# Performance work log

Measured on AMD Instinct MI355X. Metric: run time of the kernel, lower is better.

The kernel has to match this reference:

```python
import jax, jax.numpy as jnp
import numpy as np

N_SAMPLES = (16, 16)  # n_samples per layer (layer_specs)
N_MP = 2
N_HEAD = 4
BATCH = 512
N_NODES = 200000
MAX_DEG = 32
FEAT_DIM = 128
PREP_DIM = 128
HEAD_OUT = 64
ATT_HID = 128


def _agg_layer(x, nb, Wa1, wa2, Wx, Wn):
    # x: [m, d] self feats; nb: [m, S, d] neighbor feats
    # Wa1: [H, 2d, K], wa2: [H, K], Wx/Wn: [H, d, o]
    cat = jnp.concatenate([jnp.broadcast_to(x[:, None, :], nb.shape), nb], axis=-1)  # [m,S,2d]
    h = jnp.tanh(jnp.einsum('msd,hdk->mshk', cat, Wa1))          # [m,S,H,K]
    score = jnp.einsum('mshk,hk->mhs', h, wa2)                   # [m,H,S]
    alpha = jax.nn.softmax(score, axis=-1)
    agg = jnp.einsum('mhs,msd->mhd', alpha, nb)                  # [m,H,d]
    out = jax.nn.relu(jnp.einsum('md,hdo->mho', x, Wx) + jnp.einsum('mhd,hdo->mho', agg, Wn))
    return out.reshape(x.shape[0], -1)                           # concat heads -> [m, H*o]


def setup_inputs() -> dict:
    key = jax.random.key(0)
    ks = jax.random.split(key, 12)
    inp = {}
    inp['ids'] = jax.random.randint(ks[0], (BATCH,), 0, N_NODES, dtype=jnp.int32)
    inp['feats'] = jax.random.normal(ks[1], (N_NODES, FEAT_DIM), dtype=jnp.float32)
    inp['adjs'] = jax.random.randint(ks[2], (N_MP, N_NODES, MAX_DEG), 0, N_NODES, dtype=jnp.int32)
    inp['W_prep'] = jax.random.normal(ks[3], (FEAT_DIM, PREP_DIM), dtype=jnp.float32) / np.sqrt(FEAT_DIM)
    d0, d1 = PREP_DIM, N_HEAD * HEAD_OUT  # layer input dims: 128, 256
    inp['Watt1_0'] = jax.random.normal(ks[4], (N_MP, N_HEAD, 2 * d0, ATT_HID), dtype=jnp.float32) / np.sqrt(2 * d0)
    inp['watt2_0'] = jax.random.normal(ks[5], (N_MP, N_HEAD, ATT_HID), dtype=jnp.float32) / np.sqrt(ATT_HID)
    inp['Wx_0'] = jax.random.normal(ks[6], (N_MP, N_HEAD, d0, HEAD_OUT), dtype=jnp.float32) / np.sqrt(d0)
    inp['Wn_0'] = jax.random.normal(ks[7], (N_MP, N_HEAD, d0, HEAD_OUT), dtype=jnp.float32) / np.sqrt(d0)
    inp['Watt1_1'] = jax.random.normal(ks[8], (N_MP, N_HEAD, 2 * d1, ATT_HID), dtype=jnp.float32) / np.sqrt(2 * d1)
    inp['watt2_1'] = jax.random.normal(ks[9], (N_MP, N_HEAD, ATT_HID), dtype=jnp.float32) / np.sqrt(ATT_HID)
    inp['Wx_1'] = jax.random.normal(ks[10], (N_MP, N_HEAD, d1, HEAD_OUT), dtype=jnp.float32) / np.sqrt(d1)
    inp['Wn_1'] = jax.random.normal(ks[11], (N_MP, N_HEAD, d1, HEAD_OUT), dtype=jnp.float32) / np.sqrt(d1)
    return inp


def reference(ids, feats, adjs, W_prep, Watt1_0, watt2_0, Wx_0, Wn_0, Watt1_1, watt2_1, Wx_1, Wn_1):
    # eval mode (train=False): dropouts are identity
    init = feats[ids] @ W_prep  # prep(ids, feats[ids]) -> [B, 128]
    params = ((Watt1_0, watt2_0, Wx_0, Wn_0), (Watt1_1, watt2_1, Wx_1, Wn_1))
    outs = []
    for mp in range(N_MP):
        adj = adjs[mp]
        cur = ids
        all_feats = [init]
        # neighbor sampling + gather per layer (frontier: 512 -> 8192 -> 131072)
        for li, S in enumerate(N_SAMPLES):
            k = jax.random.fold_in(jax.random.key(42), mp * 16 + li)
            cols = jax.random.randint(k, (cur.shape[0], S), 0, MAX_DEG)
            cur = adj[cur[:, None], cols].reshape(-1)
            all_feats.append(feats[cur] @ W_prep)
        # depth aggregation: each layer collapses the frontier list by one level
        for li, (Wa1, wa2, Wx, Wn) in enumerate(params):
            new_feats = []
            for k_ in range(len(all_feats) - 1):
                x = all_feats[k_]
                nb = all_feats[k_ + 1].reshape(x.shape[0], N_SAMPLES[k_], -1)
                new_feats.append(_agg_layer(x, nb, Wa1[mp], wa2[mp], Wx[mp], Wn[mp]))
            all_feats = new_feats
        assert len(all_feats) == 1
        outs.append(all_feats[0])
    return jnp.stack(outs)  # [n_mp, B, n_head*head_out] = [2, 512, 256]
```

## Files before the change

kernel.cpp:

```cpp
#include <hip/hip_runtime.h>
#include <math.h>


typedef __attribute__((ext_vector_type(8))) short bf16x8;
typedef __attribute__((ext_vector_type(4))) float f32x4;

__device__ __forceinline__ float b2f(unsigned short u) {
  union { unsigned u; float f; } c; c.u = ((unsigned)u) << 16; return c.f;
}
__device__ __forceinline__ unsigned short f2b(float f) {
  union { float f; unsigned u; } c; c.f = f;
  return (unsigned short)((c.u + 0x7FFFu + ((c.u >> 16) & 1u)) >> 16);
}

__device__ __forceinline__ float fast_tanh_pre(float x) {
  float z; asm("v_exp_f32 %0, %1" : "=v"(z) : "v"(x));
  float zp1 = z + 1.f;
  float w; asm("v_rcp_f32 %0, %1" : "=v"(w) : "v"(zp1));
  return fmaf(-2.f, w, 1.f);
}
__device__ __forceinline__ float fast_exp(float x) {
  float y = x * 1.4426950408889634f;
  float z; asm("v_exp_f32 %0, %1" : "=v"(z) : "v"(y));
  return z;
}

__host__ __device__ __forceinline__ void tf2x32(unsigned k0, unsigned k1,
                                                unsigned x0, unsigned x1,
                                                unsigned& o0, unsigned& o1) {
  const unsigned ks2 = k0 ^ k1 ^ 0x1BD11BDAu;
  unsigned v0 = x0 + k0, v1 = x1 + k1;
#define TFR(r) { v0 += v1; v1 = (v1 << (r)) | (v1 >> (32 - (r))); v1 ^= v0; }
  TFR(13) TFR(15) TFR(26) TFR(6)
  v0 += k1;  v1 += ks2 + 1u;
  TFR(17) TFR(29) TFR(16) TFR(24)
  v0 += ks2; v1 += k0 + 2u;
  TFR(13) TFR(15) TFR(26) TFR(6)
  v0 += k0;  v1 += k1 + 3u;
  TFR(17) TFR(29) TFR(16) TFR(24)
  v0 += k1;  v1 += ks2 + 4u;
  TFR(13) TFR(15) TFR(26) TFR(6)
  v0 += ks2; v1 += k0 + 5u;
#undef TFR
  o0 = v0; o1 = v1;
}

__global__ void frontier2_kernel(const int* __restrict__ adjs,
                                 const int* __restrict__ ids,
                                 int* __restrict__ nodes_all,
                                 unsigned a00, unsigned a01, unsigned b00, unsigned b01,
                                 unsigned a10, unsigned a11, unsigned b10, unsigned b11) {
  const int mp = blockIdx.z;
  const int* adj = adjs + (size_t)mp * 6400000;
  int* nodes = nodes_all + (size_t)mp * 139776;
  unsigned k0a = mp ? a10 : a00, k1a = mp ? a11 : a01;
  unsigned k0b = mp ? b10 : b00, k1b = mp ? b11 : b01;
  int i = blockIdx.x * 256 + threadIdx.x;
  int j = i >> 4;
  unsigned y0, y1;
  tf2x32(k0a, k1a, 0u, (unsigned)j, y0, y1);
  int col1 = (int)((y0 ^ y1) & 31u);
  int p0 = ids[j >> 4];
  int f1 = adj[(size_t)p0 * 32 + col1];
  tf2x32(k0b, k1b, 0u, (unsigned)i, y0, y1);
  int col2 = (int)((y0 ^ y1) & 31u);
  int f2 = adj[(size_t)f1 * 32 + col2];
  nodes[8704 + i] = f2;
  if ((i & 15) == 0) nodes[512 + j] = f1;
  if (i < 512) nodes[i] = ids[i];
}

__global__ void transcast_kernel(const float* __restrict__ Wp,
                                 const float* __restrict__ Wa1_0,
                                 const float* __restrict__ Wa1_1,
                                 const float* __restrict__ Wx_0,
                                 const float* __restrict__ Wn_0,
                                 const float* __restrict__ Wx_1,
                                 const float* __restrict__ Wn_1,
                                 unsigned short* __restrict__ Wpt) {
  const float TS = 2.8853900817779268f;
  int o = blockIdx.x * 256 + threadIdx.x;
  if (o >= 1196032) return;
  float v;
  if (o < 16384) {
    int k = o & 127, c = o >> 7;
    v = Wp[k * 128 + c];
  } else if (o < 278528) {
    int o2 = o - 16384;
    int k = o2 & 127, c = (o2 >> 7) & 127, h = (o2 >> 14) & 3,
        half = (o2 >> 16) & 1, mpi = o2 >> 17;
    v = TS * Wa1_0[(((size_t)(mpi * 4 + h) * 256) + half * 128 + k) * 128 + c];
  } else if (o < 802816) {
    int o3 = o - 278528;
    int k = o3 & 255, c = (o3 >> 8) & 127, h = (o3 >> 15) & 3,
        half = (o3 >> 17) & 1, mpi = o3 >> 18;
    v = TS * Wa1_1[(((size_t)(mpi * 4 + h) * 512) + half * 256 + k) * 128 + c];
  } else if (o < 868352) {
    int o4 = o - 802816;
    int k = o4 & 127, oo = (o4 >> 7) & 63, h = (o4 >> 13) & 3, mpi = o4 >> 15;
    v = Wx_0[(((size_t)(mpi * 4 + h) * 128) + k) * 64 + oo];
  } else if (o < 933888) {
    int o4 = o - 868352;
    int k = o4 & 127, oo = (o4 >> 7) & 63, h = (o4 >> 13) & 3, mpi = o4 >> 15;
    v = Wn_0[(((size_t)(mpi * 4 + h) * 128) + k) * 64 + oo];
  } else if (o < 1064960) {
    int o5 = o - 933888;
    int k = o5 & 255, oo = (o5 >> 8) & 63, h = (o5 >> 14) & 3, mpi = o5 >> 16;
    v = Wx_1[(((size_t)(mpi * 4 + h) * 256) + k) * 64 + oo];
  } else {
    int o5 = o - 1064960;
    int k = o5 & 255, oo = (o5 >> 8) & 63, h = (o5 >> 14) & 3, mpi = o5 >> 16;
    v = Wn_1[(((size_t)(mpi * 4 + h) * 256) + k) * 64 + oo];
  }
  Wpt[o] = f2b(v);
}

template <int MODE, bool A_F32, int NKS, int MG>
__global__ __launch_bounds__(256) void mfma_gemm(
    const void* __restrict__ Av, const int* __restrict__ gather,
    const unsigned short* __restrict__ WT, void* __restrict__ Cv,
    int ldc, int mclamp, int a_str, int g_str, int w_str, int c_str) {
  constexpr int K = NKS * 32;
  const int t = threadIdx.x;
  const int w = t >> 6, l = t & 63;
  const int lr = l & 15, lg = l >> 4;
  const int hb = blockIdx.y;
  const int mp = blockIdx.z;
  const int rbase = blockIdx.x * (4 * MG * 16) + w * (MG * 16);

  const unsigned short* Wb = WT + (size_t)mp * w_str + (size_t)hb * 128 * K;
  f32x4 acc[MG][8] = {};

  int arow[MG];
#pragma unroll
  for (int mg = 0; mg < MG; ++mg) {
    int row = rbase + mg * 16 + lr;
    arow[mg] = gather ? gather[(size_t)mp * g_str + row] : min(row, mclamp);
  }
  const float* Af = (const float*)Av;
  const unsigned short* Ab = ((const unsigned short*)Av) + (size_t)mp * a_str;

#pragma unroll
  for (int ks = 0; ks < NKS; ++ks) {
    const int koff = ks * 32 + lg * 8;
    bf16x8 a[MG], b[8];
#pragma unroll
    for (int mg = 0; mg < MG; ++mg) {
      if (A_F32) {
        const float* p = Af + (size_t)arow[mg] * K + koff;
        float4 v0 = *(const float4*)p;
        float4 v1 = *(const float4*)(p + 4);
        union { short s[8]; bf16x8 v; } u;
        u.s[0] = (short)f2b(v0.x); u.s[1] = (short)f2b(v0.y);
        u.s[2] = (short)f2b(v0.z); u.s[3] = (short)f2b(v0.w);
        u.s[4] = (short)f2b(v1.x); u.s[5] = (short)f2b(v1.y);
        u.s[6] = (short)f2b(v1.z); u.s[7] = (short)f2b(v1.w);
        a[mg] = u.v;
      } else {
        a[mg] = *(const bf16x8*)(Ab + (size_t)arow[mg] * K + koff);
      }
    }
#pragma unroll
    for (int f = 0; f < 8; ++f)
      b[f] = *(const bf16x8*)(Wb + (size_t)(f * 16 + lr) * K + koff);
#pragma unroll
    for (int mg = 0; mg < MG; ++mg)
#pragma unroll
      for (int f = 0; f < 8; ++f)
        acc[mg][f] = __builtin_amdgcn_mfma_f32_16x16x32_bf16(a[mg], b[f], acc[mg][f], 0, 0, 0);
  }

  if (MODE == 0) {
    unsigned short* Cb = ((unsigned short*)Cv) + (size_t)mp * c_str;
#pragma unroll
    for (int mg = 0; mg < MG; ++mg)
#pragma unroll
      for (int f = 0; f < 8; ++f)
#pragma unroll
        for (int r = 0; r < 4; ++r)
          Cb[(size_t)(rbase + mg * 16 + lg * 4 + r) * ldc + f * 16 + lr] =
              f2b(acc[mg][f][r]);
  } else {
    float* Cf = ((float*)Cv) + (size_t)mp * c_str;
#pragma unroll
    for (int mg = 0; mg < MG; ++mg)
#pragma unroll
      for (int f = 0; f < 8; ++f)
#pragma unroll
        for (int r = 0; r < 4; ++r)
          Cf[(size_t)(rbase + mg * 16 + lg * 4 + r) * ldc + hb * 128 + f * 16 + lr] =
              acc[mg][f][r];
  }
}

template <int NKS, int MG>
__global__ __launch_bounds__(256, 2) void aggsc_mfma(
    const unsigned short* __restrict__ NB, const int* __restrict__ gather,
    const float* __restrict__ Tb, const unsigned short* __restrict__ WTbot,
    const float* __restrict__ wa2, unsigned short* __restrict__ AG,
    int nb_str, int g_str, int t_str, int w_str, int wa2_str, int ag_str) {
  constexpr int K = NKS * 32;
  constexpr int KP = K + 8;
  constexpr int ROWS = MG * 16;
  const int t = threadIdx.x;
  const int w = t >> 6, l = t & 63;
  const int lr = l & 15, lg = l >> 4;
  const int mp = blockIdx.z;
  const int rbase = blockIdx.x * ROWS;

  __shared__ unsigned short NBs[ROWS * KP];
  __shared__ float alsh[4][MG][16];

  const unsigned short* NBm = NB + (size_t)mp * nb_str;
  const int* gm = gather ? gather + (size_t)mp * g_str : nullptr;

  constexpr int CH = (ROWS * K) / (256 * 8);
#pragma unroll
  for (int q = 0; q < CH; ++q) {
    int c = q * 256 + t;
    int row = c / (K / 8), kc = c % (K / 8);
    int src = gm ? gm[rbase + row] : (rbase + row);
    bf16x8 v = *(const bf16x8*)(NBm + (size_t)src * K + kc * 8);
    *(bf16x8*)(&NBs[row * KP + kc * 8]) = v;
  }
  __syncthreads();

  const unsigned short* Wb = WTbot + (size_t)mp * w_str + (size_t)w * 128 * K;
  float sc[MG][4];
#pragma unroll
  for (int mg = 0; mg < MG; ++mg)
#pragma unroll
    for (int r = 0; r < 4; ++r) sc[mg][r] = 0.f;

#pragma unroll 1
  for (int half = 0; half < 2; ++half) {
    f32x4 acc[MG][4] = {};
#pragma unroll
    for (int ks = 0; ks < NKS; ++ks) {
      const int koff = ks * 32 + lg * 8;
      bf16x8 a[MG], b[4];
#pragma unroll
      for (int f = 0; f < 4; ++f)
        b[f] = *(const bf16x8*)(Wb + (size_t)(half * 64 + f * 16 + lr) * K + koff);
#pragma unroll
      for (int mg = 0; mg < MG; ++mg)
        a[mg] = *(const bf16x8*)(&NBs[(mg * 16 + lr) * KP + koff]);
#pragma unroll
      for (int mg = 0; mg < MG; ++mg)
#pragma unroll
        for (int f = 0; f < 4; ++f)
          acc[mg][f] = __builtin_amdgcn_mfma_f32_16x16x32_bf16(a[mg], b[f], acc[mg][f], 0, 0, 0);
    }
    float w2h[4];
#pragma unroll
    for (int f = 0; f < 4; ++f)
      w2h[f] = wa2[(size_t)mp * wa2_str + w * 128 + half * 64 + f * 16 + lr];
#pragma unroll
    for (int mg = 0; mg < MG; ++mg) {
      const int i = blockIdx.x * MG + mg;
      float tvh[4];
#pragma unroll
      for (int f = 0; f < 4; ++f)
        tvh[f] = Tb[(size_t)mp * t_str + (size_t)i * 512 + w * 128 + half * 64 + f * 16 + lr];
#pragma unroll
      for (int r = 0; r < 4; ++r) {
        float s = 0.f;
#pragma unroll
        for (int f = 0; f < 4; ++f)
          s += fast_tanh_pre(acc[mg][f][r] + tvh[f]) * w2h[f];
        sc[mg][r] += s;
      }
    }
  }

#pragma unroll
  for (int mg = 0; mg < MG; ++mg) {
    float s0 = sc[mg][0], s1 = sc[mg][1], s2 = sc[mg][2], s3 = sc[mg][3];
    s0 += __shfl_xor(s0, 1); s0 += __shfl_xor(s0, 2); s0 += __shfl_xor(s0, 4); s0 += __shfl_xor(s0, 8);
    s1 += __shfl_xor(s1, 1); s1 += __shfl_xor(s1, 2); s1 += __shfl_xor(s1, 4); s1 += __shfl_xor(s1, 8);
    s2 += __shfl_xor(s2, 1); s2 += __shfl_xor(s2, 2); s2 += __shfl_xor(s2, 4); s2 += __shfl_xor(s2, 8);
    s3 += __shfl_xor(s3, 1); s3 += __shfl_xor(s3, 2); s3 += __shfl_xor(s3, 4); s3 += __shfl_xor(s3, 8);
    float mx = fmaxf(fmaxf(s0, s1), fmaxf(s2, s3));
    mx = fmaxf(mx, __shfl_xor(mx, 16));
    mx = fmaxf(mx, __shfl_xor(mx, 32));
    float e0 = fast_exp(s0 - mx), e1 = fast_exp(s1 - mx);
    float e2 = fast_exp(s2 - mx), e3 = fast_exp(s3 - mx);
    float sum = e0 + e1 + e2 + e3;
    sum += __shfl_xor(sum, 16); sum += __shfl_xor(sum, 32);
    float inv = 1.f / sum;
    if (lr == 0) {
      alsh[w][mg][lg * 4 + 0] = e0 * inv;
      alsh[w][mg][lg * 4 + 1] = e1 * inv;
      alsh[w][mg][lg * 4 + 2] = e2 * inv;
      alsh[w][mg][lg * 4 + 3] = e3 * inv;
    }
  }

  constexpr int NCH = K >> 7;
#pragma unroll
  for (int mg = 0; mg < MG; ++mg) {
    const int i = blockIdx.x * MG + mg;
    float al[16];
#pragma unroll
    for (int s = 0; s < 16; ++s) al[s] = alsh[w][mg][s];
#pragma unroll
    for (int c = 0; c < NCH; ++c) {
      const int d = l * 2 + c * 128;
      float a0 = 0.f, a1 = 0.f;
#pragma unroll
      for (int s = 0; s < 16; ++s) {
        unsigned v = *(const unsigned*)(&NBs[(mg * 16 + s) * KP + d]);
        a0 = fmaf(al[s], b2f((unsigned short)(v & 0xffffu)), a0);
        a1 = fmaf(al[s], b2f((unsigned short)(v >> 16)), a1);
      }
      unsigned o = (unsigned)f2b(a0) | ((unsigned)f2b(a1) << 16);
      *(unsigned*)(AG + (size_t)mp * ag_str + ((size_t)i * 4 + w) * K + d) = o;
    }
  }
}

template <int DX, bool OUTB, int MG>
__global__ __launch_bounds__(256) void outg_kernel(
    const unsigned short* __restrict__ Xb, const int* __restrict__ gatherX,
    const unsigned short* __restrict__ AG,
    const unsigned short* __restrict__ WXT, const unsigned short* __restrict__ WNT,
    void* __restrict__ outv,
    int x_str, int g_str, int ag_str, int w_str, int o_str) {
  const int t = threadIdx.x;
  const int w = t >> 6, l = t & 63;
  const int lr = l & 15, lg = l >> 4;
  const int hb = blockIdx.y;
  const int mp = blockIdx.z;
  const int rbase = blockIdx.x * (4 * MG * 16) + w * (MG * 16);
  f32x4 acc[MG][4] = {};
  constexpr int nks = DX >> 5;

  const unsigned short* Xm = Xb + (size_t)mp * x_str;
  const int* gm = gatherX ? gatherX + (size_t)mp * g_str : nullptr;
  const unsigned short* AGm = AG + (size_t)mp * ag_str;
  const unsigned short* WXm = WXT + (size_t)mp * w_str;
  const unsigned short* WNm = WNT + (size_t)mp * w_str;

  int xrow[MG];
#pragma unroll
  for (int mg = 0; mg < MG; ++mg) {
    int row = rbase + mg * 16 + lr;
    xrow[mg] = gm ? gm[row] : row;
  }

#pragma unroll
  for (int ks = 0; ks < nks; ++ks) {
    const int koff = ks * 32 + lg * 8;
    bf16x8 a[MG], b[4];
#pragma unroll
    for (int mg = 0; mg < MG; ++mg)
      a[mg] = *(const bf16x8*)(Xm + (size_t)xrow[mg] * DX + koff);
#pragma unroll
    for (int f = 0; f < 4; ++f)
      b[f] = *(const bf16x8*)(WXm + (size_t)(hb * 64 + f * 16 + lr) * DX + koff);
#pragma unroll
    for (int mg = 0; mg < MG; ++mg)
#pragma unroll
      for (int f = 0; f < 4; ++f)
        acc[mg][f] = __builtin_amdgcn_mfma_f32_16x16x32_bf16(a[mg], b[f], acc[mg][f], 0, 0, 0);
  }
#pragma unroll
  for (int ks = 0; ks < nks; ++ks) {
    const int koff = ks * 32 + lg * 8;
    bf16x8 a[MG], b[4];
#pragma unroll
    for (int mg = 0; mg < MG; ++mg)
      a[mg] = *(const bf16x8*)(AGm + ((size_t)(rbase + mg * 16 + lr) * 4 + hb) * DX + koff);
#pragma unroll
    for (int f = 0; f < 4; ++f)
      b[f] = *(const bf16x8*)(WNm + (size_t)(hb * 64 + f * 16 + lr) * DX + koff);
#pragma unroll
    for (int mg = 0; mg < MG; ++mg)
#pragma unroll
      for (int f = 0; f < 4; ++f)
        acc[mg][f] = __builtin_amdgcn_mfma_f32_16x16x32_bf16(a[mg], b[f], acc[mg][f], 0, 0, 0);
  }

#pragma unroll
  for (int mg = 0; mg < MG; ++mg)
#pragma unroll
    for (int f = 0; f < 4; ++f)
#pragma unroll
      for (int r = 0; r < 4; ++r) {
        float v = fmaxf(acc[mg][f][r], 0.f);
        size_t idx = (size_t)mp * o_str +
                     (size_t)(rbase + mg * 16 + lg * 4 + r) * 256 + hb * 64 + f * 16 + lr;
        if (OUTB) ((unsigned short*)outv)[idx] = f2b(v);
        else      ((float*)outv)[idx] = v;
      }
}

extern "C" void kernel_launch(void* const* d_in, const int* in_sizes, int n_in,
                              void* d_out, int out_size, void* d_ws, size_t ws_size,
                              hipStream_t stream) {
  (void)in_sizes; (void)n_in; (void)out_size; (void)ws_size;
  const int*   ids   = (const int*)d_in[0];
  const float* feats = (const float*)d_in[1];
  const int*   adjs  = (const int*)d_in[2];
  const float* Wp    = (const float*)d_in[3];
  const float* Wa1_0 = (const float*)d_in[4];
  const float* wa2_0 = (const float*)d_in[5];
  const float* Wx_0  = (const float*)d_in[6];
  const float* Wn_0  = (const float*)d_in[7];
  const float* Wa1_1 = (const float*)d_in[8];
  const float* wa2_1 = (const float*)d_in[9];
  const float* Wx_1  = (const float*)d_in[10];
  const float* Wn_1  = (const float*)d_in[11];
  float* out = (float*)d_out;

  char* ws = (char*)d_ws;
  size_t off = 0;
  auto alloc = [&](size_t bytes) { char* p = ws + off; off += (bytes + 255) & ~(size_t)255; return p; };
  int*            nodes = (int*)alloc((size_t)2 * 139776 * 4);
  unsigned short* P_all = (unsigned short*)alloc((size_t)200064 * 128 * 2);
  float*          Tbig  = (float*)alloc((size_t)2 * 8192 * 512 * 4);
  float*          T2    = (float*)alloc((size_t)2 * 512 * 512 * 4);
  unsigned short* AGbig = (unsigned short*)alloc((size_t)2 * 8192 * 4 * 128 * 2);
  unsigned short* AG2   = (unsigned short*)alloc((size_t)2 * 512 * 4 * 256 * 2);
  unsigned short* NF1b  = (unsigned short*)alloc((size_t)2 * 8192 * 256 * 2);
  unsigned short* NF0b  = (unsigned short*)alloc((size_t)2 * 512 * 256 * 2);
  unsigned short* WB    = (unsigned short*)alloc((size_t)1196032 * 2);

  unsigned short* Wpt  = WB;
  unsigned short* WT0  = WB + 16384;
  unsigned short* WT1  = WB + 278528;
  unsigned short* WXT0 = WB + 802816;
  unsigned short* WNT0 = WB + 868352;
  unsigned short* WXT1 = WB + 933888;
  unsigned short* WNT1 = WB + 1064960;

  const int BIG = 1 << 30;

  unsigned key0[2][2], key1[2][2];
  for (int mp = 0; mp < 2; ++mp)
    for (int li = 0; li < 2; ++li) {
      unsigned K0, K1;
      tf2x32(0u, 42u, 0u, (unsigned)(mp * 16 + li), K0, K1);
      tf2x32(K0, K1, 0u, 1u, key0[mp][li], key1[mp][li]);
    }

  transcast_kernel<<<4672, 256, 0, stream>>>(Wp, Wa1_0, Wa1_1, Wx_0, Wn_0,
                                             Wx_1, Wn_1, WB);
  frontier2_kernel<<<dim3(512, 1, 2), 256, 0, stream>>>(
      adjs, ids, nodes,
      key0[0][0], key1[0][0], key0[0][1], key1[0][1],
      key0[1][0], key1[1][0], key0[1][1], key1[1][1]);

  mfma_gemm<0, true, 4, 1><<<dim3(3126, 1, 1), 256, 0, stream>>>(
      feats, nullptr, Wpt, P_all, 128, 199999, 0, 0, 0, 0);

  mfma_gemm<1, false, 4, 2><<<dim3(64, 4, 2), 256, 0, stream>>>(
      P_all, nodes + 512, WT0, Tbig, 512, BIG,
      0, 139776, 131072, 4194304);
  aggsc_mfma<4, 4><<<dim3(2048, 1, 2), 256, 0, stream>>>(
      P_all, nodes + 8704, Tbig, WT0 + 65536, wa2_0, AGbig,
      0, 139776, 4194304, 131072, 512, 4194304);
  outg_kernel<128, true, 2><<<dim3(64, 4, 2), 256, 0, stream>>>(
      P_all, nodes + 512, AGbig, WXT0, WNT0, NF1b,
      0, 139776, 4194304, 32768, 2097152);

  mfma_gemm<1, false, 4, 1><<<dim3(8, 4, 2), 256, 0, stream>>>(
      P_all, nodes, WT0, T2, 512, BIG, 0, 139776, 131072, 262144);
  aggsc_mfma<4, 2><<<dim3(256, 1, 2), 256, 0, stream>>>(
      P_all, nodes + 512, T2, WT0 + 65536, wa2_0, AG2,
      0, 139776, 262144, 131072, 512, 262144);
  outg_kernel<128, true, 1><<<dim3(8, 4, 2), 256, 0, stream>>>(
      P_all, nodes, AG2, WXT0, WNT0, NF0b, 0, 139776, 262144, 32768, 131072);

  mfma_gemm<1, false, 8, 1><<<dim3(8, 4, 2), 256, 0, stream>>>(
      NF0b, nullptr, WT1, T2, 512, 511, 131072, 0, 262144, 262144);
  aggsc_mfma<8, 2><<<dim3(256, 1, 2), 256, 0, stream>>>(
      NF1b, nullptr, T2, WT1 + 131072, wa2_1, AG2,
      2097152, 0, 262144, 262144, 512, 524288);
  outg_kernel<256, false, 1><<<dim3(8, 4, 2), 256, 0, stream>>>(
      NF0b, nullptr, AG2, WXT1, WNT1, out, 131072, 0, 524288, 65536, 131072);
}
```

Measured before the change: 285.2 us.

## Merge independent layer-0 frontier launches into split-grid kernels and vectorize AG writes

The two independent layer-0 aggregations (8192-row frontier and 512-row frontier) now share single launches of T-gemm, attention-score and output kernels, with a block-index split choosing which problem each block handles. This removes three kernel launches and lets the small problem fill idle CUs alongside the large one. The alpha-weighted aggregation epilogue is also rewritten so each lane produces eight bf16 outputs and writes them with one 128-bit store. The cost is some extra branching and register use.

```diff
diff --git a/kernel.cpp b/kernel.cpp
--- a/kernel.cpp
+++ b/kernel.cpp
@@ -194,25 +194,94 @@
 }
 
 template <int NKS, int MG>
-__global__ __launch_bounds__(256, 2) void aggsc_mfma(
-    const unsigned short* __restrict__ NB, const int* __restrict__ gather,
-    const float* __restrict__ Tb, const unsigned short* __restrict__ WTbot,
-    const float* __restrict__ wa2, unsigned short* __restrict__ AG,
-    int nb_str, int g_str, int t_str, int w_str, int wa2_str, int ag_str) {
+__global__ __launch_bounds__(256) void tgemm_m(
+    const unsigned short* __restrict__ A,
+    const int* __restrict__ g1, const int* __restrict__ g2,
+    const unsigned short* __restrict__ WT,
+    float* __restrict__ C1, float* __restrict__ C2, int split,
+    int g1_str, int g2_str, int w_str, int c1_str, int c2_str) {
+  constexpr int K = NKS * 32;
+  const int t = threadIdx.x;
+  const int w = t >> 6, l = t & 63;
+  const int lr = l & 15, lg = l >> 4;
+  const int bx = blockIdx.x, hb = blockIdx.y, mp = blockIdx.z;
+
+  const int* gm; float* Cf; int rb;
+  if (bx < split) { gm = g1 + (size_t)mp * g1_str; Cf = C1 + (size_t)mp * c1_str; rb = bx * (4 * MG * 16); }
+  else            { gm = g2 + (size_t)mp * g2_str; Cf = C2 + (size_t)mp * c2_str; rb = (bx - split) * (4 * MG * 16); }
+  const int rbase = rb + w * (MG * 16);
+
+  const unsigned short* Wb = WT + (size_t)mp * w_str + (size_t)hb * 128 * K;
+  f32x4 acc[MG][8] = {};
+
+  int arow[MG];
+#pragma unroll
+  for (int mg = 0; mg < MG; ++mg)
+    arow[mg] = gm[rbase + mg * 16 + lr];
+
+#pragma unroll
+  for (int ks = 0; ks < NKS; ++ks) {
+    const int koff = ks * 32 + lg * 8;
+    bf16x8 a[MG], b[8];
+#pragma unroll
+    for (int mg = 0; mg < MG; ++mg)
+      a[mg] = *(const bf16x8*)(A + (size_t)arow[mg] * K + koff);
+#pragma unroll
+    for (int f = 0; f < 8; ++f)
+      b[f] = *(const bf16x8*)(Wb + (size_t)(f * 16 + lr) * K + koff);
+#pragma unroll
+    for (int mg = 0; mg < MG; ++mg)
+#pragma unroll
+      for (int f = 0; f < 8; ++f)
+        acc[mg][f] = __builtin_amdgcn_mfma_f32_16x16x32_bf16(a[mg], b[f], acc[mg][f], 0, 0, 0);
+  }
+
+#pragma unroll
+  for (int mg = 0; mg < MG; ++mg)
+#pragma unroll
+    for (int f = 0; f < 8; ++f)
+#pragma unroll
+      for (int r = 0; r < 4; ++r)
+        Cf[(size_t)(rbase + mg * 16 + lg * 4 + r) * 512 + hb * 128 + f * 16 + lr] =
+            acc[mg][f][r];
+}
+
+template <int NKS, int MG>
+__global__ __launch_bounds__(256, 2) void aggsc_m(
+    const unsigned short* __restrict__ NB, int nb_str,
+    const int* __restrict__ g1, const int* __restrict__ g2,
+    const float* __restrict__ T1, const float* __restrict__ T2v,
+    const unsigned short* __restrict__ WTbot, const float* __restrict__ wa2,
+    unsigned short* __restrict__ A1, unsigned short* __restrict__ A2v, int split,
+    int g1_str, int g2_str, int t1_str, int t2_str,
+    int w_str, int wa2_str, int a1_str, int a2_str) {
   constexpr int K = NKS * 32;
   constexpr int KP = K + 8;
   constexpr int ROWS = MG * 16;
+  static_assert(MG * K == 512, "AG b128 lane mapping requires MG*K==512");
   const int t = threadIdx.x;
   const int w = t >> 6, l = t & 63;
   const int lr = l & 15, lg = l >> 4;
-  const int mp = blockIdx.z;
-  const int rbase = blockIdx.x * ROWS;
+  const int bx = blockIdx.x, mp = blockIdx.z;
+
+  const int* gm; const float* Tb; unsigned short* AG; int ib;
+  if (bx < split) {
+    gm = g1 ? g1 + (size_t)mp * g1_str : nullptr;
+    Tb = T1 + (size_t)mp * t1_str;
+    AG = A1 + (size_t)mp * a1_str;
+    ib = bx;
+  } else {
+    gm = g2 ? g2 + (size_t)mp * g2_str : nullptr;
+    Tb = T2v + (size_t)mp * t2_str;
+    AG = A2v + (size_t)mp * a2_str;
+    ib = bx - split;
+  }
+  const int rbase = ib * ROWS;
 
   __shared__ unsigned short NBs[ROWS * KP];
   __shared__ float alsh[4][MG][16];
 
   const unsigned short* NBm = NB + (size_t)mp * nb_str;
-  const int* gm = gather ? gather + (size_t)mp * g_str : nullptr;
 
   constexpr int CH = (ROWS * K) / (256 * 8);
 #pragma unroll
@@ -257,11 +326,11 @@
       w2h[f] = wa2[(size_t)mp * wa2_str + w * 128 + half * 64 + f * 16 + lr];
 #pragma unroll
     for (int mg = 0; mg < MG; ++mg) {
-      const int i = blockIdx.x * MG + mg;
+      const int i = ib * MG + mg;
       float tvh[4];
 #pragma unroll
       for (int f = 0; f < 4; ++f)
-        tvh[f] = Tb[(size_t)mp * t_str + (size_t)i * 512 + w * 128 + half * 64 + f * 16 + lr];
+        tvh[f] = Tb[(size_t)i * 512 + w * 128 + half * 64 + f * 16 + lr];
 #pragma unroll
       for (int r = 0; r < 4; ++r) {
         float s = 0.f;
@@ -296,57 +365,118 @@
     }
   }
 
-  constexpr int NCH = K >> 7;
-#pragma unroll
-  for (int mg = 0; mg < MG; ++mg) {
-    const int i = blockIdx.x * MG + mg;
-    float al[16];
-#pragma unroll
-    for (int s = 0; s < 16; ++s) al[s] = alsh[w][mg][s];
-#pragma unroll
-    for (int c = 0; c < NCH; ++c) {
-      const int d = l * 2 + c * 128;
-      float a0 = 0.f, a1 = 0.f;
-#pragma unroll
-      for (int s = 0; s < 16; ++s) {
-        unsigned v = *(const unsigned*)(&NBs[(mg * 16 + s) * KP + d]);
-        a0 = fmaf(al[s], b2f((unsigned short)(v & 0xffffu)), a0);
-        a1 = fmaf(al[s], b2f((unsigned short)(v >> 16)), a1);
-      }
-      unsigned o = (unsigned)f2b(a0) | ((unsigned)f2b(a1) << 16);
-      *(unsigned*)(AG + (size_t)mp * ag_str + ((size_t)i * 4 + w) * K + d) = o;
-    }
-  }
-}
-
-template <int DX, bool OUTB, int MG>
-__global__ __launch_bounds__(256) void outg_kernel(
-    const unsigned short* __restrict__ Xb, const int* __restrict__ gatherX,
-    const unsigned short* __restrict__ AG,
+  constexpr int LPM = 64 / MG;
+  const int mgA = l / LPM, d0 = (l % LPM) * 8;
+  const int iA = ib * MG + mgA;
+  float ad[8] = {};
+#pragma unroll
+  for (int s = 0; s < 16; ++s) {
+    float alv = alsh[w][mgA][s];
+    bf16x8 v = *(const bf16x8*)(&NBs[(mgA * 16 + s) * KP + d0]);
+#pragma unroll
+    for (int q = 0; q < 8; ++q)
+      ad[q] = fmaf(alv, b2f((unsigned short)v[q]), ad[q]);
+  }
+  union { short s[8]; bf16x8 v; } o;
+#pragma unroll
+  for (int q = 0; q < 8; ++q) o.s[q] = (short)f2b(ad[q]);
+  *(bf16x8*)(AG + ((size_t)iA * 4 + w) * K + d0) = o.v;
+}
+
+template <int DX, int MG>
+__global__ __launch_bounds__(256) void outg_m(
+    const unsigned short* __restrict__ Xb,
+    const int* __restrict__ g1, const int* __restrict__ g2,
+    const unsigned short* __restrict__ A1, const unsigned short* __restrict__ A2v,
     const unsigned short* __restrict__ WXT, const unsigned short* __restrict__ WNT,
-    void* __restrict__ outv,
-    int x_str, int g_str, int ag_str, int w_str, int o_str) {
+    unsigned short* __restrict__ O1, unsigned short* __restrict__ O2, int split,
+    int g1_str, int g2_str, int a1_str, int a2_str,
+    int w_str, int o1_str, int o2_str) {
   const int t = threadIdx.x;
   const int w = t >> 6, l = t & 63;
   const int lr = l & 15, lg = l >> 4;
-  const int hb = blockIdx.y;
-  const int mp = blockIdx.z;
+  const int bx = blockIdx.x, hb = blockIdx.y, mp = blockIdx.z;
+  constexpr int nks = DX >> 5;
+
+  const int* gm; const unsigned short* AGm; unsigned short* Om; int rb;
+  if (bx < split) {
+    gm = g1 + (size_t)mp * g1_str; AGm = A1 + (size_t)mp * a1_str;
+    Om = O1 + (size_t)mp * o1_str; rb = bx * (4 * MG * 16);
+  } else {
+    gm = g2 + (size_t)mp * g2_str; AGm = A2v + (size_t)mp * a2_str;
+    Om = O2 + (size_t)mp * o2_str; rb = (bx - split) * (4 * MG * 16);
+  }
+  const int rbase = rb + w * (MG * 16);
+  const unsigned short* WXm = WXT + (size_t)mp * w_str;
+  const unsigned short* WNm = WNT + (size_t)mp * w_str;
+  f32x4 acc[MG][4] = {};
+
+  int xrow[MG];
+#pragma unroll
+  for (int mg = 0; mg < MG; ++mg)
+    xrow[mg] = gm[rbase + mg * 16 + lr];
+
+#pragma unroll
+  for (int ks = 0; ks < nks; ++ks) {
+    const int koff = ks * 32 + lg * 8;
+    bf16x8 a[MG], b[4];
+#pragma unroll
+    for (int mg = 0; mg < MG; ++mg)
+      a[mg] = *(const bf16x8*)(Xb + (size_t)xrow[mg] * DX + koff);
+#pragma unroll
+    for (int f = 0; f < 4; ++f)
+      b[f] = *(const bf16x8*)(WXm + (size_t)(hb * 64 + f * 16 + lr) * DX + koff);
+#pragma unroll
+    for (int mg = 0; mg < MG; ++mg)
+#pragma unroll
+      for (int f = 0; f < 4; ++f)
+        acc[mg][f] = __builtin_amdgcn_mfma_f32_16x16x32_bf16(a[mg], b[f], acc[mg][f], 0, 0, 0);
+  }
+#pragma unroll
+  for (int ks = 0; ks < nks; ++ks) {
+    const int koff = ks * 32 + lg * 8;
+    bf16x8 a[MG], b[4];
+#pragma unroll
+    for (int mg = 0; mg < MG; ++mg)
+      a[mg] = *(const bf16x8*)(AGm + ((size_t)(rbase + mg * 16 + lr) * 4 + hb) * DX + koff);
+#pragma unroll
+    for (int f = 0; f < 4; ++f)
+      b[f] = *(const bf16x8*)(WNm + (size_t)(hb * 64 + f * 16 + lr) * DX + koff);
+#pragma unroll
+    for (int mg = 0; mg < MG; ++mg)
+#pragma unroll
+      for (int f = 0; f < 4; ++f)
+        acc[mg][f] = __builtin_amdgcn_mfma_f32_16x16x32_bf16(a[mg], b[f], acc[mg][f], 0, 0, 0);
+  }
+
+#pragma unroll
+  for (int mg = 0; mg < MG; ++mg)
+#pragma unroll
+    for (int f = 0; f < 4; ++f)
+#pragma unroll
+      for (int r = 0; r < 4; ++r) {
+        float v = fmaxf(acc[mg][f][r], 0.f);
+        Om[(size_t)(rbase + mg * 16 + lg * 4 + r) * 256 + hb * 64 + f * 16 + lr] = f2b(v);
+      }
+}
+
+template <int DX, int MG>
+__global__ __launch_bounds__(256) void outg_f32(
+    const unsigned short* __restrict__ Xb, const unsigned short* __restrict__ AG,
+    const unsigned short* __restrict__ WXT, const unsigned short* __restrict__ WNT,
+    float* __restrict__ outv,
+    int x_str, int ag_str, int w_str, int o_str) {
+  const int t = threadIdx.x;
+  const int w = t >> 6, l = t & 63;
+  const int lr = l & 15, lg = l >> 4;
+  const int hb = blockIdx.y, mp = blockIdx.z;
   const int rbase = blockIdx.x * (4 * MG * 16) + w * (MG * 16);
-  f32x4 acc[MG][4] = {};
   constexpr int nks = DX >> 5;
-
   const unsigned short* Xm = Xb + (size_t)mp * x_str;
-  const int* gm = gatherX ? gatherX + (size_t)mp * g_str : nullptr;
   const unsigned short* AGm = AG + (size_t)mp * ag_str;
   const unsigned short* WXm = WXT + (size_t)mp * w_str;
   const unsigned short* WNm = WNT + (size_t)mp * w_str;
-
-  int xrow[MG];
-#pragma unroll
-  for (int mg = 0; mg < MG; ++mg) {
-    int row = rbase + mg * 16 + lr;
-    xrow[mg] = gm ? gm[row] : row;
-  }
+  f32x4 acc[MG][4] = {};
 
 #pragma unroll
   for (int ks = 0; ks < nks; ++ks) {
@@ -354,7 +484,7 @@
     bf16x8 a[MG], b[4];
 #pragma unroll
     for (int mg = 0; mg < MG; ++mg)
-      a[mg] = *(const bf16x8*)(Xm + (size_t)xrow[mg] * DX + koff);
+      a[mg] = *(const bf16x8*)(Xm + (size_t)(rbase + mg * 16 + lr) * DX + koff);
 #pragma unroll
     for (int f = 0; f < 4; ++f)
       b[f] = *(const bf16x8*)(WXm + (size_t)(hb * 64 + f * 16 + lr) * DX + koff);
@@ -388,10 +518,8 @@
 #pragma unroll
       for (int r = 0; r < 4; ++r) {
         float v = fmaxf(acc[mg][f][r], 0.f);
-        size_t idx = (size_t)mp * o_str +
-                     (size_t)(rbase + mg * 16 + lg * 4 + r) * 256 + hb * 64 + f * 16 + lr;
-        if (OUTB) ((unsigned short*)outv)[idx] = f2b(v);
-        else      ((float*)outv)[idx] = v;
+        outv[(size_t)mp * o_str +
+             (size_t)(rbase + mg * 16 + lg * 4 + r) * 256 + hb * 64 + f * 16 + lr] = v;
       }
 }
 
@@ -434,8 +562,6 @@
   unsigned short* WXT1 = WB + 933888;
   unsigned short* WNT1 = WB + 1064960;
 
-  const int BIG = 1 << 30;
-
   unsigned key0[2][2], key1[2][2];
   for (int mp = 0; mp < 2; ++mp)
     for (int li = 0; li < 2; ++li) {
@@ -454,29 +580,22 @@
   mfma_gemm<0, true, 4, 1><<<dim3(3126, 1, 1), 256, 0, stream>>>(
       feats, nullptr, Wpt, P_all, 128, 199999, 0, 0, 0, 0);
 
-  mfma_gemm<1, false, 4, 2><<<dim3(64, 4, 2), 256, 0, stream>>>(
-      P_all, nodes + 512, WT0, Tbig, 512, BIG,
-      0, 139776, 131072, 4194304);
-  aggsc_mfma<4, 4><<<dim3(2048, 1, 2), 256, 0, stream>>>(
-      P_all, nodes + 8704, Tbig, WT0 + 65536, wa2_0, AGbig,
-      0, 139776, 4194304, 131072, 512, 4194304);
-  outg_kernel<128, true, 2><<<dim3(64, 4, 2), 256, 0, stream>>>(
-      P_all, nodes + 512, AGbig, WXT0, WNT0, NF1b,
-      0, 139776, 4194304, 32768, 2097152);
-
-  mfma_gemm<1, false, 4, 1><<<dim3(8, 4, 2), 256, 0, stream>>>(
-      P_all, nodes, WT0, T2, 512, BIG, 0, 139776, 131072, 262144);
-  aggsc_mfma<4, 2><<<dim3(256, 1, 2), 256, 0, stream>>>(
-      P_all, nodes + 512, T2, WT0 + 65536, wa2_0, AG2,
-      0, 139776, 262144, 131072, 512, 262144);
-  outg_kernel<128, true, 1><<<dim3(8, 4, 2), 256, 0, stream>>>(
-      P_all, nodes, AG2, WXT0, WNT0, NF0b, 0, 139776, 262144, 32768, 131072);
+  tgemm_m<4, 2><<<dim3(68, 4, 2), 256, 0, stream>>>(
+      P_all, nodes + 512, nodes, WT0, Tbig, T2, 64,
+      139776, 139776, 131072, 4194304, 262144);
+  aggsc_m<4, 4><<<dim3(2176, 1, 2), 256, 0, stream>>>(
+      P_all, 0, nodes + 8704, nodes + 512, Tbig, T2, WT0 + 65536, wa2_0,
+      AGbig, AG2, 2048, 139776, 139776, 4194304, 262144, 131072, 512,
+      4194304, 262144);
+  outg_m<128, 2><<<dim3(68, 4, 2), 256, 0, stream>>>(
+      P_all, nodes + 512, nodes, AGbig, AG2, WXT0, WNT0, NF1b, NF0b, 64,
+      139776, 139776, 4194304, 262144, 32768, 2097152, 131072);
 
   mfma_gemm<1, false, 8, 1><<<dim3(8, 4, 2), 256, 0, stream>>>(
       NF0b, nullptr, WT1, T2, 512, 511, 131072, 0, 262144, 262144);
-  aggsc_mfma<8, 2><<<dim3(256, 1, 2), 256, 0, stream>>>(
-      NF1b, nullptr, T2, WT1 + 131072, wa2_1, AG2,
-      2097152, 0, 262144, 262144, 512, 524288);
-  outg_kernel<256, false, 1><<<dim3(8, 4, 2), 256, 0, stream>>>(
-      NF0b, nullptr, AG2, WXT1, WNT1, out, 131072, 0, 524288, 65536, 131072);
-}
+  aggsc_m<8, 2><<<dim3(256, 1, 2), 256, 0, stream>>>(
+      NF1b, 2097152, nullptr, nullptr, T2, T2, WT1 + 131072, wa2_1,
+      AG2, AG2, 256, 0, 0, 262144, 262144, 262144, 512, 524288, 524288);
+  outg_f32<256, 1><<<dim3(8, 4, 2), 256, 0, stream>>>(
+      NF0b, AG2, WXT1, WNT1, out, 131072, 524288, 65536, 131072);
+}
```

Result: faster. 272.4 us (-4.5%).
